# Kernel tuning notes

Measured on AMD Instinct MI355X. Metric: run time of the kernel, lower is better.

Reference implementation:

```python
import jax, jax.numpy as jnp
import numpy as np

U, T, K, Q, H = 4096, 200, 64, 10000, 128
STD_THETA = 1.0


def setup_inputs() -> dict:
    key = jax.random.key(0)
    ks = jax.random.split(key, 12)
    q_id = jax.random.randint(ks[0], (U, T), 0, Q, dtype=jnp.int32)
    resp = jax.random.randint(ks[1], (U, T), 0, 2, dtype=jnp.int32)
    # one KC per question so the per-timestep masked_select size is constant (= U)
    kc_of_q = jax.random.randint(ks[2], (Q,), 0, K)
    kmap = jax.nn.one_hot(kc_of_q, K, dtype=jnp.float32) > 0.5  # (Q, K) bool, one-hot
    mask = jnp.ones((U, T), dtype=bool)
    diff_mu = jax.random.normal(ks[3], (Q,), dtype=jnp.float32)
    disc_mu = jax.random.normal(ks[4], (Q,), dtype=jnp.float32)
    xav = lambda k, fi, fo: jax.random.normal(k, (fi, fo), dtype=jnp.float32) * (2.0 / (fi + fo)) ** 0.5
    W1 = xav(ks[5], 3, H)
    W2 = xav(ks[6], H, H)
    W3 = xav(ks[7], H, 2)
    b1 = jnp.zeros((H,), jnp.float32)
    b2 = jnp.zeros((H,), jnp.float32)
    b3 = jnp.zeros((2,), jnp.float32)
    return dict(mask=mask, q_id=q_id, kmap=kmap, resp=resp,
                diff_mu=diff_mu, disc_mu=disc_mu,
                W1=W1, b1=b1, W2=W2, b2=b2, W3=W3, b3=b3)


def reference(mask, q_id, kmap, resp, diff_mu, disc_mu, W1, b1, W2, b2, W3, b3):
    gelu = lambda x: jax.nn.gelu(x, approximate=False)  # torch nn.GELU default = exact erf
    nu = q_id.shape[0]
    td = diff_mu[q_id]                      # (U, T) trial difficulty
    ts = disc_mu[q_id]                      # (U, T) trial discrimination
    x = jnp.stack([td, ts, resp.astype(jnp.float32)], axis=-1)  # (U, T, 3)
    h = gelu(gelu(x @ W1 + b1) @ W2 + b2)
    out = gelu(h @ W3 + b3)                 # (U, T, 2)
    mu = out[..., 0].T                      # (T, U)
    logvar = out[..., 1].T                  # (T, U)
    std = jnp.maximum(jnp.exp(0.5 * logvar), 1e-8)
    r = (STD_THETA / std) ** 2              # (T, U)

    # backward Kalman-style recursion: b_t = 1/(1 + r_t + (1 - b_{t+1})), c_t = b_t*(c_{t+1} + r_t*mu_t)
    def bwd_step(carry, rm):
        b_n, c_n = carry
        r_t, mu_t = rm
        b_t = 1.0 / (1.0 + r_t + (1.0 - b_n))
        c_t = b_t * (c_n + r_t * mu_t)
        return (b_t, c_t), (b_t, c_t)

    init = (jnp.ones((nu,), mu.dtype), jnp.zeros((nu,), mu.dtype))
    _, (b_seq, c_seq) = jax.lax.scan(bwd_step, init, (r, mu), reverse=True)  # (T, U) each

    # forward pass: gather active-KC ability, update, scatter back into per-user KC state
    active_kc = jnp.argmax(kmap[q_id], axis=-1).T  # (T, U) one active KC per trial
    uidx = jnp.arange(nu)

    def fwd_step(curr, bck):
        b_t, c_t, kc_t = bck
        prev = curr[uidx, kc_t]
        mu_t = b_t * prev + c_t
        curr = curr.at[uidx, kc_t].set(mu_t)
        return curr, mu_t

    curr0 = jnp.zeros((nu, kmap.shape[1]), mu.dtype)
    last_ability_kc, ability_T = jax.lax.scan(fwd_step, curr0, (b_seq, c_seq, active_kc))
    ability = ability_T.T                   # (U, T): masked mean over one-hot KC = active KC ability
    trial_logits = ts * (ability - td)      # (U, T)
    return trial_logits, last_ability_kc
```

## Files before the change

kernel.cpp:

```cpp
#include <hip/hip_runtime.h>
#include <math.h>

#define U_ 4096
#define T_ 200
#define K_ 64
#define Q_ 10000
#define H_ 128
#define UPB 16

__device__ __forceinline__ float gelu_f(float x) {
  return 0.5f * x * (1.0f + erff(x * 0.70710678118654752440f));
}

__global__ __launch_bounds__(256, 4) void mlp_table_kernel(
    const float* __restrict__ diff_mu, const float* __restrict__ disc_mu,
    const float* __restrict__ W1, const float* __restrict__ b1,
    const float* __restrict__ W2, const float* __restrict__ b2,
    const float* __restrict__ W3, const float* __restrict__ b3,
    const unsigned char* __restrict__ kmap,
    float4* __restrict__ tab4, int* __restrict__ kc_of_q) {
  __shared__ float W2s[64 * H_];
  __shared__ float h1buf[16][H_];

  const int tid = threadIdx.x;
  const int base = blockIdx.x * 16;

  for (int v = tid; v < 64 * H_; v += 256) W2s[v] = W2[v];

  if (blockIdx.x < 40) {
    int q = blockIdx.x * 256 + tid;
    if (q < Q_) {
      const unsigned char* km = kmap + (size_t)q * K_;
      int kc = 0;
#pragma unroll
      for (int k = 0; k < K_; ++k)
        if (km[k]) kc = k;
      kc_of_q[q] = kc;
    }
  }

  for (int v = tid; v < 16 * H_; v += 256) {
    int pl = v >> 7, j = v & 127;
    int pg = base + pl;
    int q = pg >> 1;
    float rf = (float)(pg & 1);
    float td = diff_mu[q], ts = disc_mu[q];
    float a = b1[j];
    a += td * W1[j];
    a += ts * W1[H_ + j];
    a += rf * W1[2 * H_ + j];
    h1buf[pl][j] = gelu_f(a);
  }
  __syncthreads();

  const int w = tid >> 6, lane = tid & 63;
  float a0[4] = {0.f, 0.f, 0.f, 0.f}, a1[4] = {0.f, 0.f, 0.f, 0.f};
  const float* h1w = &h1buf[w * 4][0];

#pragma clang loop unroll_count(8)
  for (int k = 0; k < 64; ++k) {
    float w0 = W2s[k * H_ + lane];
    float w1 = W2s[k * H_ + lane + 64];
#pragma unroll
    for (int p = 0; p < 4; ++p) {
      float hv = h1w[p * H_ + k];
      a0[p] = fmaf(w0, hv, a0[p]);
      a1[p] = fmaf(w1, hv, a1[p]);
    }
  }
  __syncthreads();
  for (int v = tid; v < 64 * H_; v += 256) W2s[v] = W2[64 * H_ + v];
  __syncthreads();
#pragma clang loop unroll_count(8)
  for (int k = 0; k < 64; ++k) {
    float w0 = W2s[k * H_ + lane];
    float w1 = W2s[k * H_ + lane + 64];
#pragma unroll
    for (int p = 0; p < 4; ++p) {
      float hv = h1w[p * H_ + 64 + k];
      a0[p] = fmaf(w0, hv, a0[p]);
      a1[p] = fmaf(w1, hv, a1[p]);
    }
  }

  float w30a = W3[lane * 2 + 0], w31a = W3[lane * 2 + 1];
  float w30b = W3[(lane + 64) * 2 + 0], w31b = W3[(lane + 64) * 2 + 1];
  float b2a = b2[lane], b2b = b2[lane + 64];
  float b30 = b3[0], b31 = b3[1];
#pragma unroll
  for (int p = 0; p < 4; ++p) {
    float h2a = gelu_f(a0[p] + b2a);
    float h2b = gelu_f(a1[p] + b2b);
    float s0 = h2a * w30a + h2b * w30b;
    float s1 = h2a * w31a + h2b * w31b;
#pragma unroll
    for (int off = 32; off > 0; off >>= 1) {
      s0 += __shfl_xor(s0, off, 64);
      s1 += __shfl_xor(s1, off, 64);
    }
    if (lane == 0) {
      float mu = gelu_f(s0 + b30);
      float lv = gelu_f(s1 + b31);
      float sd = fmaxf(expf(0.5f * lv), 1e-8f);
      int pg = base + w * 4 + p;
      int q = pg >> 1;
      tab4[pg] = make_float4(1.0f / (sd * sd), mu, disc_mu[q], diff_mu[q]);
    }
  }
}

__global__ __launch_bounds__(256) void scan2_kernel(
    const int* __restrict__ q_id, const int* __restrict__ resp,
    const float4* __restrict__ tab4, const int* __restrict__ kc_of_q,
    float* __restrict__ out) {
  __shared__ float2 bcs[T_ * (UPB + 1)];
  __shared__ unsigned char kcs[T_ * UPB];
  __shared__ float states[UPB * (K_ + 1)];

  const int tid = threadIdx.x;
  const int lane = tid & 63;
  const int wv = tid >> 6;
  const int u0 = blockIdx.x * UPB;

  for (int v = tid; v < UPB * (K_ + 1); v += 256) states[v] = 0.0f;

  for (int uu = 0; uu < 4; ++uu) {
    const int ul = wv * 4 + uu;
    const int* qrow = q_id + (size_t)(u0 + ul) * T_;
    const int* rrow = resp + (size_t)(u0 + ul) * T_;
#pragma unroll
    for (int tile = 0; tile < 4; ++tile) {
      int t = tile * 64 + lane;
      if (t < T_) {
        int q = qrow[t];
        int rp = rrow[t];
        float4 f = tab4[q * 2 + rp];
        bcs[t * (UPB + 1) + ul] = make_float2(f.x, f.y);
        kcs[t * UPB + ul] = (unsigned char)kc_of_q[q];
      }
    }
  }
  __syncthreads();

  if (wv == 0) {
    const bool act = lane < UPB;
    const int ll = act ? lane : 0;

    float b = 1.0f, c = 0.0f;
#pragma unroll 4
    for (int t = T_ - 1; t >= 0; --t) {
      float2 rm_ = bcs[t * (UPB + 1) + ll];
      float x_ = 2.0f + rm_.x - b;
      float ib = __builtin_amdgcn_rcpf(x_);
      ib = ib * (2.0f - x_ * ib);
      b = ib;
      c = b * fmaf(rm_.x, rm_.y, c);
      if (act) bcs[t * (UPB + 1) + lane] = make_float2(b, c);
    }

#pragma unroll 2
    for (int t = 0; t < T_; ++t) {
      float2 bc_ = bcs[t * (UPB + 1) + ll];
      int kc = (int)kcs[t * UPB + ll];
      float prev = states[ll * (K_ + 1) + kc];
      float ab = fmaf(bc_.x, prev, bc_.y);
      if (act) {
        states[lane * (K_ + 1) + kc] = ab;
        bcs[t * (UPB + 1) + lane].x = ab;
      }
    }
  }
  __syncthreads();

  float* logits = out;
  float* last = out + (size_t)U_ * T_;

  for (int ul = 0; ul < UPB; ++ul) {
    if (tid < T_) {
      const int gu = u0 + ul;
      int q = q_id[(size_t)gu * T_ + tid];
      int rp = resp[(size_t)gu * T_ + tid];
      float4 f = tab4[q * 2 + rp];
      float ab = bcs[tid * (UPB + 1) + ul].x;
      logits[(size_t)gu * T_ + tid] = f.z * (ab - f.w);
    }
  }
  for (int v = tid; v < UPB * K_; v += 256) {
    int ul = v >> 6, kc = v & 63;
    last[(size_t)(u0 + ul) * K_ + kc] = states[ul * (K_ + 1) + kc];
  }
}

extern "C" void kernel_launch(void* const* d_in, const int* in_sizes, int n_in,
                              void* d_out, int out_size, void* d_ws,
                              size_t ws_size, hipStream_t stream) {
  const int* q_id = (const int*)d_in[1];
  const unsigned char* kmap = (const unsigned char*)d_in[2];
  const int* resp = (const int*)d_in[3];
  const float* diff_mu = (const float*)d_in[4];
  const float* disc_mu = (const float*)d_in[5];
  const float* W1 = (const float*)d_in[6];
  const float* b1 = (const float*)d_in[7];
  const float* W2 = (const float*)d_in[8];
  const float* b2 = (const float*)d_in[9];
  const float* W3 = (const float*)d_in[10];
  const float* b3 = (const float*)d_in[11];
  float* out = (float*)d_out;
  char* ws = (char*)d_ws;

  auto align512 = [](size_t x) { return (x + 511) & ~(size_t)511; };
  size_t o = 0;
  float4* tab4 = (float4*)(ws + o);  o = align512(o + (size_t)2 * Q_ * 16);
  int* kc_of_q = (int*)(ws + o);     o = align512(o + (size_t)Q_ * 4);
  (void)ws_size; (void)in_sizes; (void)n_in; (void)out_size;

  mlp_table_kernel<<<1250, 256, 0, stream>>>(diff_mu, disc_mu, W1, b1, W2, b2,
                                             W3, b3, kmap, tab4, kc_of_q);
  scan2_kernel<<<U_ / UPB, 256, 0, stream>>>(q_id, resp, tab4, kc_of_q, out);
}
```

Measured before the change: 141.1 us.

## Spread forward KC-state scan across a wavefront per user with register-held state

The scan kernel now assigns one 64-lane wavefront per user, with 8 users per 512-thread block. In the forward pass each lane holds one knowledge-component state in a register and updates it only when the active KC matches its lane. This removes the shared-memory state array and the serialized gather/scatter done by a single wave. Logit parameters are kept in registers from the load phase instead of being re-gathered from global memory. The backward recursion still runs on one wave, now over fewer users per block, and every lane of a wave walks all 200 timesteps.

```diff
diff --git a/kernel.cpp b/kernel.cpp
--- a/kernel.cpp
+++ b/kernel.cpp
@@ -6,7 +6,7 @@
 #define K_ 64
 #define Q_ 10000
 #define H_ 128
-#define UPB 16
+#define UPB 8
 
 __device__ __forceinline__ float gelu_f(float x) {
   return 0.5f * x * (1.0f + erff(x * 0.70710678118654752440f));
@@ -109,45 +109,41 @@
   }
 }
 
-__global__ __launch_bounds__(256) void scan2_kernel(
+__global__ __launch_bounds__(512) void scan2_kernel(
     const int* __restrict__ q_id, const int* __restrict__ resp,
     const float4* __restrict__ tab4, const int* __restrict__ kc_of_q,
     float* __restrict__ out) {
   __shared__ float2 bcs[T_ * (UPB + 1)];
   __shared__ unsigned char kcs[T_ * UPB];
-  __shared__ float states[UPB * (K_ + 1)];
 
   const int tid = threadIdx.x;
   const int lane = tid & 63;
-  const int wv = tid >> 6;
-  const int u0 = blockIdx.x * UPB;
-
-  for (int v = tid; v < UPB * (K_ + 1); v += 256) states[v] = 0.0f;
-
-  for (int uu = 0; uu < 4; ++uu) {
-    const int ul = wv * 4 + uu;
-    const int* qrow = q_id + (size_t)(u0 + ul) * T_;
-    const int* rrow = resp + (size_t)(u0 + ul) * T_;
-#pragma unroll
-    for (int tile = 0; tile < 4; ++tile) {
-      int t = tile * 64 + lane;
-      if (t < T_) {
-        int q = qrow[t];
-        int rp = rrow[t];
-        float4 f = tab4[q * 2 + rp];
-        bcs[t * (UPB + 1) + ul] = make_float2(f.x, f.y);
-        kcs[t * UPB + ul] = (unsigned char)kc_of_q[q];
-      }
-    }
-  }
-  __syncthreads();
-
-  if (wv == 0) {
+  const int ul = tid >> 6;
+  const int gu = blockIdx.x * UPB + ul;
+
+  float tts[4], ttd[4];
+  const int* qrow = q_id + (size_t)gu * T_;
+  const int* rrow = resp + (size_t)gu * T_;
+#pragma unroll
+  for (int tile = 0; tile < 4; ++tile) {
+    int t = tile * 64 + lane;
+    if (t < T_) {
+      int q = qrow[t];
+      int rp = rrow[t];
+      float4 f = tab4[q * 2 + rp];
+      bcs[t * (UPB + 1) + ul] = make_float2(f.x, f.y);
+      kcs[t * UPB + ul] = (unsigned char)kc_of_q[q];
+      tts[tile] = f.z;
+      ttd[tile] = f.w;
+    }
+  }
+  __syncthreads();
+
+  if (tid < 64) {
     const bool act = lane < UPB;
     const int ll = act ? lane : 0;
-
     float b = 1.0f, c = 0.0f;
-#pragma unroll 4
+#pragma unroll 8
     for (int t = T_ - 1; t >= 0; --t) {
       float2 rm_ = bcs[t * (UPB + 1) + ll];
       float x_ = 2.0f + rm_.x - b;
@@ -157,38 +153,32 @@
       c = b * fmaf(rm_.x, rm_.y, c);
       if (act) bcs[t * (UPB + 1) + lane] = make_float2(b, c);
     }
-
-#pragma unroll 2
-    for (int t = 0; t < T_; ++t) {
-      float2 bc_ = bcs[t * (UPB + 1) + ll];
-      int kc = (int)kcs[t * UPB + ll];
-      float prev = states[ll * (K_ + 1) + kc];
-      float ab = fmaf(bc_.x, prev, bc_.y);
-      if (act) {
-        states[lane * (K_ + 1) + kc] = ab;
-        bcs[t * (UPB + 1) + lane].x = ab;
-      }
-    }
+  }
+  __syncthreads();
+
+  float x = 0.0f;
+#pragma unroll 8
+  for (int t = 0; t < T_; ++t) {
+    float2 bc_ = bcs[t * (UPB + 1) + ul];
+    int kc = (int)kcs[t * UPB + ul];
+    float xn = fmaf(bc_.x, x, bc_.y);
+    bool hit = (lane == kc);
+    x = hit ? xn : x;
+    if (hit) bcs[t * (UPB + 1) + ul].x = xn;
   }
   __syncthreads();
 
   float* logits = out;
   float* last = out + (size_t)U_ * T_;
-
-  for (int ul = 0; ul < UPB; ++ul) {
-    if (tid < T_) {
-      const int gu = u0 + ul;
-      int q = q_id[(size_t)gu * T_ + tid];
-      int rp = resp[(size_t)gu * T_ + tid];
-      float4 f = tab4[q * 2 + rp];
-      float ab = bcs[tid * (UPB + 1) + ul].x;
-      logits[(size_t)gu * T_ + tid] = f.z * (ab - f.w);
-    }
-  }
-  for (int v = tid; v < UPB * K_; v += 256) {
-    int ul = v >> 6, kc = v & 63;
-    last[(size_t)(u0 + ul) * K_ + kc] = states[ul * (K_ + 1) + kc];
-  }
+#pragma unroll
+  for (int tile = 0; tile < 4; ++tile) {
+    int t = tile * 64 + lane;
+    if (t < T_) {
+      float ab = bcs[t * (UPB + 1) + ul].x;
+      logits[(size_t)gu * T_ + t] = tts[tile] * (ab - ttd[tile]);
+    }
+  }
+  last[(size_t)gu * K_ + lane] = x;
 }
 
 extern "C" void kernel_launch(void* const* d_in, const int* in_sizes, int n_in,
@@ -216,5 +206,5 @@
 
   mlp_table_kernel<<<1250, 256, 0, stream>>>(diff_mu, disc_mu, W1, b1, W2, b2,
                                              W3, b3, kmap, tab4, kc_of_q);
-  scan2_kernel<<<U_ / UPB, 256, 0, stream>>>(q_id, resp, tab4, kc_of_q, out);
-}
+  scan2_kernel<<<U_ / UPB, 512, 0, stream>>>(q_id, resp, tab4, kc_of_q, out);
+}
```

Result: faster. 137.0 us (-2.9%).
